# Performance work log

Hardware: AMD Instinct MI355X
Metric: run time of the kernel (lower is better)

The kernel has to match this reference:

```python
import jax, jax.numpy as jnp
import numpy as np

N = 16384   # number of samples (sample_idx.shape[0])
H = 512     # hidden_size
D = 128     # input_size
K = 40      # number of observation times
E = 4096    # events per observation time (event_pt blocks made uniform)
DT = 0.05
STEPS_PER_OBS = 2   # obs_times = 2*dt*(1..K) -> exactly 2 Euler steps per obs
EXTRA_STEPS = 10    # prop_to_end Euler steps after last obs (no effect on loss)


def setup_inputs() -> dict:
    key = jax.random.key(0)
    ks = jax.random.split(key, 16)

    X = jax.random.normal(ks[0], (K, E, D), dtype=jnp.float32)
    M = (jax.random.uniform(ks[1], (K, E, D)) < 0.8).astype(jnp.float32)
    # unique sample indices per observation block (torch index-assign assumes
    # no duplicate rows within one event block)
    batch_idx = jax.vmap(lambda k: jax.random.permutation(k, N)[:E])(
        jax.random.split(ks[2], K)).astype(jnp.int32)

    def xavier(k, shape):
        fan_in, fan_out = shape[1], shape[0]
        lim = np.sqrt(6.0 / (fan_in + fan_out))
        return jax.random.uniform(k, shape, jnp.float32, -lim, lim)

    b = lambda n: jnp.full((n,), 0.01, jnp.float32)  # torch bias fill 0.01

    return {
        "X": X, "M": M, "batch_idx": batch_idx,
        # RNNCell params (torch layout: W_ih [H,D], W_hh [H,H])
        "W_ih": xavier(ks[3], (H, D)), "b_ih": b(H),
        "W_hh": xavier(ks[4], (H, H)), "b_hh": b(H),
        # ODEFunc: Linear(H,H) -> tanh -> Linear(H,H)
        "Wo1": xavier(ks[5], (H, H)), "bo1": b(H),
        "Wo2": xavier(ks[6], (H, H)), "bo2": b(H),
        # p_model: Linear(H,H) -> ReLU -> (Dropout p=0, eval) -> Linear(H,D)
        "Wp1": xavier(ks[7], (H, H)), "bp1": b(H),
        "Wp2": xavier(ks[8], (D, H)), "bp2": b(D),
    }


def reference(X, M, batch_idx, W_ih, b_ih, W_hh, b_hh,
              Wo1, bo1, Wo2, bo2, Wp1, bp1, Wp2, bp2):
    def euler(h):
        # h + dt * ODEFunc(h)
        dh = jnp.tanh(h @ Wo1.T + bo1) @ Wo2.T + bo2
        return h + DT * dh

    def p_model(h):
        return jax.nn.relu(h @ Wp1.T + bp1) @ Wp2.T + bp2

    def obs_step(carry, inp):
        h, loss, tot_m = carry
        X_obs, M_obs, i_obs = inp  # [E,D], [E,D], [E]
        # Euler propagation up to this observation time
        for _ in range(STEPS_PER_OBS):
            h = euler(h)
        # MAE loss against prediction p = p_model(h) at observed samples
        p_obs = p_model(h[i_obs])
        loss = loss + jnp.sum(jnp.abs(X_obs - p_obs) * M_obs)
        tot_m = tot_m + jnp.sum(M_obs)
        # RNNCell update (tanh) scattered back into observed rows
        h_new = jnp.tanh(X_obs @ W_ih.T + b_ih + h[i_obs] @ W_hh.T + b_hh)
        h = h.at[i_obs].set(h_new)
        return (h, loss, tot_m), None

    h0 = jnp.zeros((N, H), X.dtype)
    zero = jnp.zeros((), X.dtype)
    (h, loss, tot_m), _ = jax.lax.scan(obs_step, (h0, zero, zero),
                                       (X, M, batch_idx))
    # prop_to_end: extra Euler steps (does not change the returned losses)
    h = jax.lax.fori_loop(0, EXTRA_STEPS, lambda i, hh: euler(hh), h)
    # original returns (loss, loss / total_M_obs); stacked for convenience
    return jnp.stack([loss, loss / tot_m])
```

## Files before the change

kernel.cpp:

```cpp
#include <hip/hip_runtime.h>
#include <hip/hip_bf16.h>
#include <cstddef>
#include <cstdint>

#define NS   16384
#define HS   512
#define DS   128
#define KOBS 40
#define ES   4096
#define DTC  0.05f

typedef __bf16 bf16x8 __attribute__((ext_vector_type(8)));
typedef float  f32x4  __attribute__((ext_vector_type(4)));
typedef __hip_bfloat16 bf16_t;

__device__ __forceinline__ void async16(const void* g, void* l)
{
  __builtin_amdgcn_global_load_lds(
      (const __attribute__((address_space(1))) unsigned int*)g,
      (__attribute__((address_space(3))) unsigned int*)l, 16, 0, 0);
}

__device__ __forceinline__ float fast_tanh(float x)
{
  return 1.f - 2.f / (1.f + __expf(2.f * x));
}

template <int IT, int JT>
__device__ __forceinline__ void mfma_half(
    f32x4 (&acc)[IT][JT], const bf16_t* Ah, const bf16_t* Bh,
    int wr, int wc, int q, int ln)
{
  bf16x8 a[IT], b[JT];
#pragma unroll
  for (int i = 0; i < IT; ++i)
    a[i] = *(const bf16x8*)(Ah + (wr + i * 16 + ln) * 32 + q * 8);
#pragma unroll
  for (int j = 0; j < JT; ++j)
    b[j] = *(const bf16x8*)(Bh + (wc + j * 16 + ln) * 32 + q * 8);
#pragma unroll
  for (int i = 0; i < IT; ++i)
#pragma unroll
    for (int j = 0; j < JT; ++j)
      acc[i][j] = __builtin_amdgcn_mfma_f32_16x16x32_bf16(a[i], b[j], acc[i][j], 0, 0, 0);
}

__device__ __forceinline__ void loop128(
    f32x4 (&acc)[4][4],
    const bf16_t* __restrict__ A, int lda, const int* __restrict__ idx, int row0,
    const bf16_t* __restrict__ W, int ldw, int col0, int K,
    bf16_t* As, bf16_t* Bs)
{
  const int tid = threadIdx.x, wave = tid >> 6, lane = tid & 63;
  const int q = lane >> 4, ln = lane & 15;
  const int wr = (wave >> 1) * 64, wc = (wave & 1) * 64;
  const int srow = wave * 16 + (lane >> 2);
  const int skc  = (lane & 3) * 8;
  int ar0 = row0 + srow, ar1 = row0 + srow + 64;
  if (idx) { ar0 = idx[ar0]; ar1 = idx[ar1]; }
  const bf16_t* Ap0 = A + (size_t)ar0 * lda + skc;
  const bf16_t* Ap1 = A + (size_t)ar1 * lda + skc;
  const bf16_t* Bp0 = W + (size_t)(col0 + srow) * ldw + skc;
  const bf16_t* Bp1 = W + (size_t)(col0 + srow + 64) * ldw + skc;
  const int d0 = srow * 32 + skc, d1 = (srow + 64) * 32 + skc;

  for (int k0 = 0; k0 < K; k0 += 128) {
    __syncthreads();
#pragma unroll
    for (int s = 0; s < 4; ++s) {
      async16(Ap0 + k0 + s * 32, As + s * 4096 + d0);
      async16(Ap1 + k0 + s * 32, As + s * 4096 + d1);
      async16(Bp0 + k0 + s * 32, Bs + s * 4096 + d0);
      async16(Bp1 + k0 + s * 32, Bs + s * 4096 + d1);
    }
    __syncthreads();
#pragma unroll
    for (int s = 0; s < 4; ++s)
      mfma_half<4, 4>(acc, As + s * 4096, Bs + s * 4096, wr, wc, q, ln);
  }
}

__device__ __forceinline__ void loop64(
    f32x4 (&acc)[2][2],
    const bf16_t* __restrict__ A, int lda, int row0,
    const bf16_t* __restrict__ W, int ldw, int col0, int K,
    bf16_t* As, bf16_t* Bs)
{
  const int tid = threadIdx.x, wave = tid >> 6, lane = tid & 63;
  const int q = lane >> 4, ln = lane & 15;
  const int wr = (wave >> 1) * 32, wc = (wave & 1) * 32;
  const int srow = tid >> 2;
  const int skc  = (tid & 3) * 8;
  const bf16_t* Ap = A + (size_t)(row0 + srow) * lda + skc;
  const bf16_t* Bp = W + (size_t)(col0 + srow) * ldw + skc;
  bf16_t* As0 = As;           bf16_t* As1 = As + 64 * 32;
  bf16_t* Bs0 = Bs;           bf16_t* Bs1 = Bs + 64 * 32;
  const int d = srow * 32 + skc;

  for (int k0 = 0; k0 < K; k0 += 64) {
    __syncthreads();
    async16(Ap + k0,      As0 + d);
    async16(Bp + k0,      Bs0 + d);
    async16(Ap + k0 + 32, As1 + d);
    async16(Bp + k0 + 32, Bs1 + d);
    __syncthreads();
    mfma_half<2, 2>(acc, As0, Bs0, wr, wc, q, ln);
    mfma_half<2, 2>(acc, As1, Bs1, wr, wc, q, ln);
  }
}

__device__ __forceinline__ void gemm_k512(
    f32x4 (&acc)[4][4], const char* Tb, const bf16_t* __restrict__ Wf,
    int wc, int q, int ln)
{
  const int abase = ln * 1024;
  const int l3 = ln & 7;
  const bf16_t* Wl = Wf + (q * 512 + wc + ln) * 8;
  bf16x8 wA[4], wB[4];
#pragma unroll
  for (int i = 0; i < 4; ++i) wA[i] = *(const bf16x8*)(Wl + i * 128);
#pragma unroll 1
  for (int ks2 = 0; ks2 < 8; ++ks2) {
    {
      const bf16_t* Wk = Wl + (2 * ks2 + 1) * 16384;
#pragma unroll
      for (int i = 0; i < 4; ++i) wB[i] = *(const bf16x8*)(Wk + i * 128);
    }
    {
      bf16x8 t[4];
      const int coff = (((2 * ks2) * 4 + q) ^ l3) << 4;
#pragma unroll
      for (int jb = 0; jb < 4; ++jb)
        t[jb] = *(const bf16x8*)(Tb + jb * 16384 + abase + coff);
#pragma unroll
      for (int i = 0; i < 4; ++i)
#pragma unroll
        for (int jb = 0; jb < 4; ++jb)
          acc[i][jb] = __builtin_amdgcn_mfma_f32_16x16x32_bf16(wA[i], t[jb], acc[i][jb], 0, 0, 0);
    }
    if (ks2 < 7) {
      const bf16_t* Wk = Wl + (2 * ks2 + 2) * 16384;
#pragma unroll
      for (int i = 0; i < 4; ++i) wA[i] = *(const bf16x8*)(Wk + i * 128);
    }
    {
      bf16x8 t[4];
      const int coff = (((2 * ks2 + 1) * 4 + q) ^ l3) << 4;
#pragma unroll
      for (int jb = 0; jb < 4; ++jb)
        t[jb] = *(const bf16x8*)(Tb + jb * 16384 + abase + coff);
#pragma unroll
      for (int i = 0; i < 4; ++i)
#pragma unroll
        for (int jb = 0; jb < 4; ++jb)
          acc[i][jb] = __builtin_amdgcn_mfma_f32_16x16x32_bf16(wB[i], t[jb], acc[i][jb], 0, 0, 0);
    }
  }
}

__global__ __launch_bounds__(512)
__attribute__((amdgpu_waves_per_eu(2, 2)))
void k_euler2(
    bf16_t* __restrict__ h,
    const bf16_t* __restrict__ Wo1, const float* __restrict__ bo1,
    const bf16_t* __restrict__ Wo2, const float* __restrict__ bo2)
{
  __shared__ __align__(16) char Hs[64 * 1024];
  __shared__ __align__(16) char Ts[64 * 1024];
  const int tid = threadIdx.x;
  const int wave = tid >> 6, lane = tid & 63;
  const int q = lane >> 4, ln = lane & 15;
  const int wc = wave * 64;
  const int r0 = blockIdx.x * 64;

#pragma unroll
  for (int u = 0; u < 8; ++u) {
    const int g = u * 512 + tid;
    const int row = g >> 6, c16 = g & 63;
    *(uint4*)(Hs + row * 1024 + ((c16 ^ (row & 7)) << 4)) =
        *(const uint4*)(h + (size_t)(r0 + row) * HS + c16 * 8);
  }
  __syncthreads();

#pragma unroll 1
  for (int step = 0; step < 2; ++step) {
    {
      f32x4 acc[4][4] = {};
      gemm_k512(acc, Hs, Wo1, wc, q, ln);
#pragma unroll
      for (int i = 0; i < 4; ++i) {
        const int c0 = wc + i * 16 + q * 4;
        const float4 b4 = *(const float4*)(bo1 + c0);
        const int cb = c0 * 2;
#pragma unroll
        for (int jb = 0; jb < 4; ++jb) {
          const int row = jb * 16 + ln;
          __attribute__((aligned(8))) bf16_t pk[4];
          pk[0] = __float2bfloat16(fast_tanh(acc[i][jb][0] + b4.x));
          pk[1] = __float2bfloat16(fast_tanh(acc[i][jb][1] + b4.y));
          pk[2] = __float2bfloat16(fast_tanh(acc[i][jb][2] + b4.z));
          pk[3] = __float2bfloat16(fast_tanh(acc[i][jb][3] + b4.w));
          *(uint2*)(Ts + row * 1024 + (((cb >> 4) ^ (row & 7)) << 4) + (cb & 15)) =
              *(const uint2*)pk;
        }
      }
    }
    __syncthreads();
    {
      f32x4 acc[4][4] = {};
      gemm_k512(acc, Ts, Wo2, wc, q, ln);
#pragma unroll
      for (int i = 0; i < 4; ++i) {
        const int c0 = wc + i * 16 + q * 4;
        const float4 b4 = *(const float4*)(bo2 + c0);
        const int cb = c0 * 2;
#pragma unroll
        for (int jb = 0; jb < 4; ++jb) {
          const int row = jb * 16 + ln;
          char* p = Hs + row * 1024 + (((cb >> 4) ^ (row & 7)) << 4) + (cb & 15);
          uint2 ov = *(const uint2*)p;
          const bf16_t* ob = (const bf16_t*)&ov;
          __attribute__((aligned(8))) bf16_t pk[4];
          pk[0] = __float2bfloat16(__bfloat162float(ob[0]) + DTC * (acc[i][jb][0] + b4.x));
          pk[1] = __float2bfloat16(__bfloat162float(ob[1]) + DTC * (acc[i][jb][1] + b4.y));
          pk[2] = __float2bfloat16(__bfloat162float(ob[2]) + DTC * (acc[i][jb][2] + b4.z));
          pk[3] = __float2bfloat16(__bfloat162float(ob[3]) + DTC * (acc[i][jb][3] + b4.w));
          *(uint2*)p = *(const uint2*)pk;
        }
      }
    }
    __syncthreads();
  }

#pragma unroll
  for (int u = 0; u < 8; ++u) {
    const int g = u * 512 + tid;
    const int row = g >> 6, c16 = g & 63;
    *(uint4*)(h + (size_t)(r0 + row) * HS + c16 * 8) =
        *(const uint4*)(Hs + row * 1024 + ((c16 ^ (row & 7)) << 4));
  }
}

__global__ __launch_bounds__(256) void k_obs_pre(
    const bf16_t* __restrict__ h, const int* __restrict__ idx,
    const bf16_t* __restrict__ Wp1, const float* __restrict__ bp1,
    bf16_t* __restrict__ tmpE,
    const float* __restrict__ Xk,
    const bf16_t* __restrict__ Wih, const float* __restrict__ b_ih,
    const bf16_t* __restrict__ Whh, const float* __restrict__ b_hh,
    bf16_t* __restrict__ hnewE)
{
  __shared__ bf16_t As[128 * 128], Bs[128 * 128];
  f32x4 acc[4][4] = {};
  const int tid = threadIdx.x, wave = tid >> 6, lane = tid & 63;
  const int q = lane >> 4, ln = lane & 15;
  const int wr = (wave >> 1) * 64, wc = (wave & 1) * 64;
  const int row0 = blockIdx.x * 128, col0 = blockIdx.y * 128;

  if (blockIdx.z == 0) {
    loop128(acc, h, HS, idx, row0, Wp1, HS, col0, HS, As, Bs);
#pragma unroll
    for (int j = 0; j < 4; ++j) {
      const int c = col0 + wc + j * 16 + ln;
      const float bj = bp1[c];
#pragma unroll
      for (int i = 0; i < 4; ++i)
#pragma unroll
        for (int r = 0; r < 4; ++r) {
          const int rw = row0 + wr + i * 16 + q * 4 + r;
          const float v = acc[i][j][r] + bj;
          tmpE[(size_t)rw * HS + c] = __float2bfloat16(v > 0.f ? v : 0.f);
        }
    }
  } else {
    {
      const int srow = wave * 16 + (lane >> 2);
      const int skc  = (lane & 3) * 8;
      const bf16_t* Bp0 = Wih + (size_t)(col0 + srow) * DS + skc;
      const bf16_t* Bp1 = Wih + (size_t)(col0 + srow + 64) * DS + skc;
      const int d0 = srow * 32 + skc, d1 = (srow + 64) * 32 + skc;
      const int xr = tid >> 1, xh = (tid & 1) * 16;
#pragma unroll
      for (int s = 0; s < 4; ++s) {
        async16(Bp0 + s * 32, Bs + s * 4096 + d0);
        async16(Bp1 + s * 32, Bs + s * 4096 + d1);
      }
#pragma unroll
      for (int s = 0; s < 4; ++s) {
        const float* src = Xk + (size_t)(row0 + xr) * DS + s * 32 + xh;
        __attribute__((aligned(16))) bf16_t buf[16];
#pragma unroll
        for (int u = 0; u < 16; ++u) buf[u] = __float2bfloat16(src[u]);
        *(uint4*)(As + s * 4096 + xr * 32 + xh)     = *(const uint4*)buf;
        *(uint4*)(As + s * 4096 + xr * 32 + xh + 8) = *(const uint4*)(buf + 8);
      }
      __syncthreads();
#pragma unroll
      for (int s = 0; s < 4; ++s)
        mfma_half<4, 4>(acc, As + s * 4096, Bs + s * 4096, wr, wc, q, ln);
    }
    loop128(acc, h, HS, idx, row0, Whh, HS, col0, HS, As, Bs);
#pragma unroll
    for (int j = 0; j < 4; ++j) {
      const int c = col0 + wc + j * 16 + ln;
      const float bj = b_ih[c] + b_hh[c];
#pragma unroll
      for (int i = 0; i < 4; ++i)
#pragma unroll
        for (int r = 0; r < 4; ++r) {
          const int rw = row0 + wr + i * 16 + q * 4 + r;
          hnewE[(size_t)rw * HS + c] = __float2bfloat16(fast_tanh(acc[i][j][r] + bj));
        }
    }
  }
}

__global__ __launch_bounds__(256) void k_obs_post(
    const bf16_t* __restrict__ tmpE, const bf16_t* __restrict__ Wp2,
    const float* __restrict__ bp2, const float* __restrict__ X,
    const float* __restrict__ Mm, float* __restrict__ accum,
    bf16_t* __restrict__ h, const bf16_t* __restrict__ hnewE,
    const int* __restrict__ idx)
{
  const int bid = blockIdx.x;
  if (bid >= 128) {
    const int t  = (bid - 128) * 256 + threadIdx.x;
    const int r  = t >> 6;
    const int c8 = (t & 63) * 8;
    const int gr = idx[r];
    *(uint4*)(h + (size_t)gr * HS + c8) = *(const uint4*)(hnewE + (size_t)r * HS + c8);
    return;
  }
  __shared__ bf16_t As[64 * 64], Bs[64 * 64];
  f32x4 acc[2][2] = {};
  const int wave = threadIdx.x >> 6, lane = threadIdx.x & 63;
  const int q = lane >> 4, ln = lane & 15;
  const int wr = (wave >> 1) * 32, wc = (wave & 1) * 32;
  const int row0 = (bid >> 1) * 64, col0 = (bid & 1) * 64;
  loop64(acc, tmpE, HS, row0, Wp2, HS, col0, HS, As, Bs);
  float ls = 0.f;
#pragma unroll
  for (int j = 0; j < 2; ++j) {
    const int c = col0 + wc + j * 16 + ln;
    const float bj = bp2[c];
#pragma unroll
    for (int i = 0; i < 2; ++i)
#pragma unroll
      for (int r = 0; r < 4; ++r) {
        const int rw = row0 + wr + i * 16 + q * 4 + r;
        const float p = acc[i][j][r] + bj;
        const size_t o = (size_t)rw * DS + c;
        ls += fabsf(X[o] - p) * Mm[o];
      }
  }
#pragma unroll
  for (int off = 32; off > 0; off >>= 1) ls += __shfl_down(ls, off);
  __shared__ float red[4];
  if (lane == 0) red[wave] = ls;
  __syncthreads();
  if (threadIdx.x == 0) atomicAdd(accum, red[0] + red[1] + red[2] + red[3]);
}

__global__ void k_cvt(const float* __restrict__ s, bf16_t* __restrict__ d, int n)
{
  const int i = blockIdx.x * 256 + threadIdx.x;
  if (i * 4 < n) {
    const float4 v = ((const float4*)s)[i];
    d[i * 4 + 0] = __float2bfloat16(v.x);
    d[i * 4 + 1] = __float2bfloat16(v.y);
    d[i * 4 + 2] = __float2bfloat16(v.z);
    d[i * 4 + 3] = __float2bfloat16(v.w);
  }
}

__global__ void k_cvt_frag(const float* __restrict__ s, bf16_t* __restrict__ d)
{
  const int t = blockIdx.x * 256 + threadIdx.x;
  const int r = t & 511, c = t >> 9;
  const float4 v0 = *(const float4*)(s + (size_t)r * HS + c * 8);
  const float4 v1 = *(const float4*)(s + (size_t)r * HS + c * 8 + 4);
  __attribute__((aligned(16))) bf16_t buf[8];
  buf[0] = __float2bfloat16(v0.x); buf[1] = __float2bfloat16(v0.y);
  buf[2] = __float2bfloat16(v0.z); buf[3] = __float2bfloat16(v0.w);
  buf[4] = __float2bfloat16(v1.x); buf[5] = __float2bfloat16(v1.y);
  buf[6] = __float2bfloat16(v1.z); buf[7] = __float2bfloat16(v1.w);
  *(uint4*)(d + (size_t)t * 8) = *(const uint4*)buf;
}

__global__ void k_zero(float* __restrict__ p, size_t n4)
{
  size_t i = (size_t)blockIdx.x * blockDim.x + threadIdx.x;
  const size_t st = (size_t)gridDim.x * blockDim.x;
  const float4 z = {0.f, 0.f, 0.f, 0.f};
  for (; i < n4; i += st) ((float4*)p)[i] = z;
}

__global__ void k_zero_accum(float* accum)
{
  if (threadIdx.x < 2) accum[threadIdx.x] = 0.f;
}

__global__ void k_sum(const float* __restrict__ M, size_t n4, float* __restrict__ accum)
{
  __shared__ float red[256];
  float s = 0.f;
  for (size_t i = (size_t)blockIdx.x * blockDim.x + threadIdx.x; i < n4;
       i += (size_t)gridDim.x * blockDim.x) {
    const float4 v = ((const float4*)M)[i];
    s += v.x + v.y + v.z + v.w;
  }
  red[threadIdx.x] = s;
  __syncthreads();
  for (int st = 128; st > 0; st >>= 1) {
    if (threadIdx.x < st) red[threadIdx.x] += red[threadIdx.x + st];
    __syncthreads();
  }
  if (threadIdx.x == 0) atomicAdd(accum + 1, red[0]);
}

__global__ void k_final(const float* __restrict__ accum, float* __restrict__ out)
{
  out[0] = accum[0];
  out[1] = accum[0] / accum[1];
}

extern "C" void kernel_launch(void* const* d_in, const int* in_sizes, int n_in,
                              void* d_out, int out_size, void* d_ws, size_t ws_size,
                              hipStream_t stream)
{
  const float* X    = (const float*)d_in[0];
  const float* M    = (const float*)d_in[1];
  const int*   bidx = (const int*)d_in[2];
  const float* W_ih = (const float*)d_in[3];
  const float* b_ih = (const float*)d_in[4];
  const float* W_hh = (const float*)d_in[5];
  const float* b_hh = (const float*)d_in[6];
  const float* Wo1  = (const float*)d_in[7];
  const float* bo1  = (const float*)d_in[8];
  const float* Wo2  = (const float*)d_in[9];
  const float* bo2  = (const float*)d_in[10];
  const float* Wp1  = (const float*)d_in[11];
  const float* bp1  = (const float*)d_in[12];
  const float* Wp2  = (const float*)d_in[13];
  const float* bp2  = (const float*)d_in[14];
  float* out = (float*)d_out;

  char* w = (char*)d_ws;
  bf16_t* h     = (bf16_t*)w;                         w += (size_t)NS * HS * 2;
  bf16_t* tmpE  = (bf16_t*)w;                         w += (size_t)ES * HS * 2;
  bf16_t* hnewE = (bf16_t*)w;                         w += (size_t)ES * HS * 2;
  bf16_t* wWo1  = (bf16_t*)w;                         w += (size_t)HS * HS * 2;
  bf16_t* wWo2  = (bf16_t*)w;                         w += (size_t)HS * HS * 2;
  bf16_t* wWp1  = (bf16_t*)w;                         w += (size_t)HS * HS * 2;
  bf16_t* wWp2  = (bf16_t*)w;                         w += (size_t)DS * HS * 2;
  bf16_t* wWih  = (bf16_t*)w;                         w += (size_t)HS * DS * 2;
  bf16_t* wWhh  = (bf16_t*)w;                         w += (size_t)HS * HS * 2;
  float*  accum = (float*)w;

  k_zero<<<2048, 256, 0, stream>>>((float*)h, (size_t)NS * HS * 2 / 16);
  k_zero_accum<<<1, 64, 0, stream>>>(accum);
  k_sum<<<2048, 256, 0, stream>>>(M, (size_t)KOBS * ES * DS / 4, accum);
  k_cvt_frag<<<128, 256, 0, stream>>>(Wo1, wWo1);
  k_cvt_frag<<<128, 256, 0, stream>>>(Wo2, wWo2);
  k_cvt<<<256, 256, 0, stream>>>(Wp1, wWp1, HS * HS);
  k_cvt<<<64, 256, 0, stream>>>(Wp2, wWp2, DS * HS);
  k_cvt<<<64, 256, 0, stream>>>(W_ih, wWih, HS * DS);
  k_cvt<<<256, 256, 0, stream>>>(W_hh, wWhh, HS * HS);

  const dim3 gPre(ES / 128, HS / 128, 2);
  const int  gPost = 128 + ES * HS / 8 / 256;

  for (int k = 0; k < KOBS; ++k) {
    const int*   idx = bidx + (size_t)k * ES;
    const float* Xk  = X + (size_t)k * ES * DS;
    const float* Mk  = M + (size_t)k * ES * DS;

    k_euler2<<<NS / 64, 512, 0, stream>>>(h, wWo1, bo1, wWo2, bo2);
    k_obs_pre <<<gPre, 256, 0, stream>>>(h, idx, wWp1, bp1, tmpE,
                                         Xk, wWih, b_ih, wWhh, b_hh, hnewE);
    k_obs_post<<<gPost, 256, 0, stream>>>(tmpE, wWp2, bp2, Xk, Mk, accum,
                                          h, hnewE, idx);
  }

  k_final<<<1, 1, 0, stream>>>(accum, out);
}
```

Before: 2.853 ms.

## Halve column tiles in obs GEMMs and raise MFMA wave priority in euler

The obs_pre tile shrinks from 128x128 to 128x64 and the obs_post tile from 64x64 to 64x32, which doubles the number of blocks in both launches. The goal is to fill more of the device's compute units on these small event-sized GEMMs. The cost is that each A row tile is loaded twice as often and each block does less MFMA work per load. Separately, the euler GEMM wraps its MFMA bursts in s_setprio so those waves get issue priority over waves that are loading.

```diff
diff --git a/kernel.cpp b/kernel.cpp
--- a/kernel.cpp
+++ b/kernel.cpp
@@ -45,24 +45,25 @@
       acc[i][j] = __builtin_amdgcn_mfma_f32_16x16x32_bf16(a[i], b[j], acc[i][j], 0, 0, 0);
 }
 
-__device__ __forceinline__ void loop128(
-    f32x4 (&acc)[4][4],
-    const bf16_t* __restrict__ A, int lda, const int* __restrict__ idx, int row0,
+__device__ __forceinline__ void loop_pre(
+    f32x4 (&acc)[4][2],
+    const bf16_t* __restrict__ A, const int* __restrict__ idx, int row0,
     const bf16_t* __restrict__ W, int ldw, int col0, int K,
     bf16_t* As, bf16_t* Bs)
 {
   const int tid = threadIdx.x, wave = tid >> 6, lane = tid & 63;
   const int q = lane >> 4, ln = lane & 15;
-  const int wr = (wave >> 1) * 64, wc = (wave & 1) * 64;
+  const int wr = (wave >> 1) * 64, wc = (wave & 1) * 32;
   const int srow = wave * 16 + (lane >> 2);
   const int skc  = (lane & 3) * 8;
   int ar0 = row0 + srow, ar1 = row0 + srow + 64;
   if (idx) { ar0 = idx[ar0]; ar1 = idx[ar1]; }
-  const bf16_t* Ap0 = A + (size_t)ar0 * lda + skc;
-  const bf16_t* Ap1 = A + (size_t)ar1 * lda + skc;
-  const bf16_t* Bp0 = W + (size_t)(col0 + srow) * ldw + skc;
-  const bf16_t* Bp1 = W + (size_t)(col0 + srow + 64) * ldw + skc;
+  const bf16_t* Ap0 = A + (size_t)ar0 * HS + skc;
+  const bf16_t* Ap1 = A + (size_t)ar1 * HS + skc;
+  const int brow = tid >> 2;
+  const bf16_t* Bp = W + (size_t)(col0 + brow) * ldw + skc;
   const int d0 = srow * 32 + skc, d1 = (srow + 64) * 32 + skc;
+  const int db = brow * 32 + skc;
 
   for (int k0 = 0; k0 < K; k0 += 128) {
     __syncthreads();
@@ -70,42 +71,43 @@
     for (int s = 0; s < 4; ++s) {
       async16(Ap0 + k0 + s * 32, As + s * 4096 + d0);
       async16(Ap1 + k0 + s * 32, As + s * 4096 + d1);
-      async16(Bp0 + k0 + s * 32, Bs + s * 4096 + d0);
-      async16(Bp1 + k0 + s * 32, Bs + s * 4096 + d1);
+      async16(Bp  + k0 + s * 32, Bs + s * 2048 + db);
     }
     __syncthreads();
 #pragma unroll
     for (int s = 0; s < 4; ++s)
-      mfma_half<4, 4>(acc, As + s * 4096, Bs + s * 4096, wr, wc, q, ln);
-  }
-}
-
-__device__ __forceinline__ void loop64(
-    f32x4 (&acc)[2][2],
-    const bf16_t* __restrict__ A, int lda, int row0,
-    const bf16_t* __restrict__ W, int ldw, int col0, int K,
+      mfma_half<4, 2>(acc, As + s * 4096, Bs + s * 2048, wr, wc, q, ln);
+  }
+}
+
+__device__ __forceinline__ void loop_post(
+    f32x4 (&acc)[2][1],
+    const bf16_t* __restrict__ A, int row0,
+    const bf16_t* __restrict__ W, int col0, int K,
     bf16_t* As, bf16_t* Bs)
 {
   const int tid = threadIdx.x, wave = tid >> 6, lane = tid & 63;
   const int q = lane >> 4, ln = lane & 15;
-  const int wr = (wave >> 1) * 32, wc = (wave & 1) * 32;
+  const int wr = (wave >> 1) * 32, wc = (wave & 1) * 16;
   const int srow = tid >> 2;
   const int skc  = (tid & 3) * 8;
-  const bf16_t* Ap = A + (size_t)(row0 + srow) * lda + skc;
-  const bf16_t* Bp = W + (size_t)(col0 + srow) * ldw + skc;
-  bf16_t* As0 = As;           bf16_t* As1 = As + 64 * 32;
-  bf16_t* Bs0 = Bs;           bf16_t* Bs1 = Bs + 64 * 32;
+  const bf16_t* Ap = A + (size_t)(row0 + srow) * HS + skc;
   const int d = srow * 32 + skc;
+  const int brow = (tid & 127) >> 2;
+  const bf16_t* Bp = W + (size_t)(col0 + brow) * HS + skc;
+  const int dbB = brow * 32 + skc;
 
   for (int k0 = 0; k0 < K; k0 += 64) {
     __syncthreads();
-    async16(Ap + k0,      As0 + d);
-    async16(Bp + k0,      Bs0 + d);
-    async16(Ap + k0 + 32, As1 + d);
-    async16(Bp + k0 + 32, Bs1 + d);
-    __syncthreads();
-    mfma_half<2, 2>(acc, As0, Bs0, wr, wc, q, ln);
-    mfma_half<2, 2>(acc, As1, Bs1, wr, wc, q, ln);
+    async16(Ap + k0,      As + d);
+    async16(Ap + k0 + 32, As + 2048 + d);
+    if (tid < 128) {
+      async16(Bp + k0,      Bs + dbB);
+      async16(Bp + k0 + 32, Bs + 1024 + dbB);
+    }
+    __syncthreads();
+    mfma_half<2, 1>(acc, As,        Bs,        wr, wc, q, ln);
+    mfma_half<2, 1>(acc, As + 2048, Bs + 1024, wr, wc, q, ln);
   }
 }
 
@@ -132,11 +134,13 @@
 #pragma unroll
       for (int jb = 0; jb < 4; ++jb)
         t[jb] = *(const bf16x8*)(Tb + jb * 16384 + abase + coff);
+      __builtin_amdgcn_s_setprio(1);
 #pragma unroll
       for (int i = 0; i < 4; ++i)
 #pragma unroll
         for (int jb = 0; jb < 4; ++jb)
           acc[i][jb] = __builtin_amdgcn_mfma_f32_16x16x32_bf16(wA[i], t[jb], acc[i][jb], 0, 0, 0);
+      __builtin_amdgcn_s_setprio(0);
     }
     if (ks2 < 7) {
       const bf16_t* Wk = Wl + (2 * ks2 + 2) * 16384;
@@ -149,11 +153,13 @@
 #pragma unroll
       for (int jb = 0; jb < 4; ++jb)
         t[jb] = *(const bf16x8*)(Tb + jb * 16384 + abase + coff);
+      __builtin_amdgcn_s_setprio(1);
 #pragma unroll
       for (int i = 0; i < 4; ++i)
 #pragma unroll
         for (int jb = 0; jb < 4; ++jb)
           acc[i][jb] = __builtin_amdgcn_mfma_f32_16x16x32_bf16(wB[i], t[jb], acc[i][jb], 0, 0, 0);
+      __builtin_amdgcn_s_setprio(0);
     }
   }
 }
@@ -250,17 +256,17 @@
     const bf16_t* __restrict__ Whh, const float* __restrict__ b_hh,
     bf16_t* __restrict__ hnewE)
 {
-  __shared__ bf16_t As[128 * 128], Bs[128 * 128];
-  f32x4 acc[4][4] = {};
+  __shared__ bf16_t As[128 * 128], Bs[64 * 128];
+  f32x4 acc[4][2] = {};
   const int tid = threadIdx.x, wave = tid >> 6, lane = tid & 63;
   const int q = lane >> 4, ln = lane & 15;
-  const int wr = (wave >> 1) * 64, wc = (wave & 1) * 64;
-  const int row0 = blockIdx.x * 128, col0 = blockIdx.y * 128;
+  const int wr = (wave >> 1) * 64, wc = (wave & 1) * 32;
+  const int row0 = blockIdx.x * 128, col0 = blockIdx.y * 64;
 
   if (blockIdx.z == 0) {
-    loop128(acc, h, HS, idx, row0, Wp1, HS, col0, HS, As, Bs);
-#pragma unroll
-    for (int j = 0; j < 4; ++j) {
+    loop_pre(acc, h, idx, row0, Wp1, HS, col0, HS, As, Bs);
+#pragma unroll
+    for (int j = 0; j < 2; ++j) {
       const int c = col0 + wc + j * 16 + ln;
       const float bj = bp1[c];
 #pragma unroll
@@ -274,17 +280,14 @@
     }
   } else {
     {
-      const int srow = wave * 16 + (lane >> 2);
-      const int skc  = (lane & 3) * 8;
-      const bf16_t* Bp0 = Wih + (size_t)(col0 + srow) * DS + skc;
-      const bf16_t* Bp1 = Wih + (size_t)(col0 + srow + 64) * DS + skc;
-      const int d0 = srow * 32 + skc, d1 = (srow + 64) * 32 + skc;
+      const int brow = tid >> 2;
+      const int skc  = (tid & 3) * 8;
+      const bf16_t* Bp = Wih + (size_t)(col0 + brow) * DS + skc;
+      const int db = brow * 32 + skc;
       const int xr = tid >> 1, xh = (tid & 1) * 16;
 #pragma unroll
-      for (int s = 0; s < 4; ++s) {
-        async16(Bp0 + s * 32, Bs + s * 4096 + d0);
-        async16(Bp1 + s * 32, Bs + s * 4096 + d1);
-      }
+      for (int s = 0; s < 4; ++s)
+        async16(Bp + s * 32, Bs + s * 2048 + db);
 #pragma unroll
       for (int s = 0; s < 4; ++s) {
         const float* src = Xk + (size_t)(row0 + xr) * DS + s * 32 + xh;
@@ -297,11 +300,11 @@
       __syncthreads();
 #pragma unroll
       for (int s = 0; s < 4; ++s)
-        mfma_half<4, 4>(acc, As + s * 4096, Bs + s * 4096, wr, wc, q, ln);
-    }
-    loop128(acc, h, HS, idx, row0, Whh, HS, col0, HS, As, Bs);
-#pragma unroll
-    for (int j = 0; j < 4; ++j) {
+        mfma_half<4, 2>(acc, As + s * 4096, Bs + s * 2048, wr, wc, q, ln);
+    }
+    loop_pre(acc, h, idx, row0, Whh, HS, col0, HS, As, Bs);
+#pragma unroll
+    for (int j = 0; j < 2; ++j) {
       const int c = col0 + wc + j * 16 + ln;
       const float bj = b_ih[c] + b_hh[c];
 #pragma unroll
@@ -323,32 +326,31 @@
     const int* __restrict__ idx)
 {
   const int bid = blockIdx.x;
-  if (bid >= 128) {
-    const int t  = (bid - 128) * 256 + threadIdx.x;
+  if (bid >= 256) {
+    const int t  = (bid - 256) * 256 + threadIdx.x;
     const int r  = t >> 6;
     const int c8 = (t & 63) * 8;
     const int gr = idx[r];
     *(uint4*)(h + (size_t)gr * HS + c8) = *(const uint4*)(hnewE + (size_t)r * HS + c8);
     return;
   }
-  __shared__ bf16_t As[64 * 64], Bs[64 * 64];
-  f32x4 acc[2][2] = {};
+  __shared__ bf16_t As[64 * 64], Bs[32 * 64];
+  f32x4 acc[2][1] = {};
   const int wave = threadIdx.x >> 6, lane = threadIdx.x & 63;
   const int q = lane >> 4, ln = lane & 15;
-  const int wr = (wave >> 1) * 32, wc = (wave & 1) * 32;
-  const int row0 = (bid >> 1) * 64, col0 = (bid & 1) * 64;
-  loop64(acc, tmpE, HS, row0, Wp2, HS, col0, HS, As, Bs);
+  const int wr = (wave >> 1) * 32, wc = (wave & 1) * 16;
+  const int row0 = (bid >> 2) * 64, col0 = (bid & 3) * 32;
+  loop_post(acc, tmpE, row0, Wp2, col0, HS, As, Bs);
   float ls = 0.f;
-#pragma unroll
-  for (int j = 0; j < 2; ++j) {
-    const int c = col0 + wc + j * 16 + ln;
+  {
+    const int c = col0 + wc + ln;
     const float bj = bp2[c];
 #pragma unroll
     for (int i = 0; i < 2; ++i)
 #pragma unroll
       for (int r = 0; r < 4; ++r) {
         const int rw = row0 + wr + i * 16 + q * 4 + r;
-        const float p = acc[i][j][r] + bj;
+        const float p = acc[i][0][r] + bj;
         const size_t o = (size_t)rw * DS + c;
         ls += fabsf(X[o] - p) * Mm[o];
       }
@@ -467,8 +469,8 @@
   k_cvt<<<64, 256, 0, stream>>>(W_ih, wWih, HS * DS);
   k_cvt<<<256, 256, 0, stream>>>(W_hh, wWhh, HS * HS);
 
-  const dim3 gPre(ES / 128, HS / 128, 2);
-  const int  gPost = 128 + ES * HS / 8 / 256;
+  const dim3 gPre(ES / 128, HS / 64, 2);
+  const int  gPost = 256 + ES * HS / 8 / 256;
 
   for (int k = 0; k < KOBS; ++k) {
     const int*   idx = bidx + (size_t)k * ES;
```

Result: faster. 2.793 ms (-2.1%).
